# Performance work log

Measured on AMD Instinct MI355X. Metric: run time of the kernel, lower is better.

## Reference

```python
import jax, jax.numpy as jnp
import numpy as np

TAIL_BOUND = 20.0  # B
NUM_BINS = 16      # K
G, I = 8, 64       # n_gaussians, n_inputs
BATCH = 16384


def _rqs_forward(x, W, H, D, B):
    """Monotonic rational-quadratic spline (Durkan et al.), forward direction.
    x: [Bt,G,I]; W,H: [G,I,K] logits; D: [G,I,K-1] raw derivatives.
    Matches torch module: widths/heights = 2*B*softmax(logits), derivs = softplus,
    boundary derivatives fixed to 1, identity outside [-B, B].
    """
    dt = x.dtype
    widths = 2.0 * B * jax.nn.softmax(W, axis=-1)          # [G,I,K], sums to 2B
    heights = 2.0 * B * jax.nn.softmax(H, axis=-1)
    g, i, K = widths.shape
    one = jnp.ones((g, i, 1), dt)
    derivs = jnp.concatenate([one, jax.nn.softplus(D), one], axis=-1)  # [G,I,K+1]
    negB = jnp.full((g, i, 1), -B, dt)
    cumw = jnp.concatenate([negB, -B + jnp.cumsum(widths, -1)], -1)    # [G,I,K+1] knot x
    cumh = jnp.concatenate([negB, -B + jnp.cumsum(heights, -1)], -1)   # [G,I,K+1] knot y
    delta = heights / widths                                            # bin slopes

    inside = (x >= -B) & (x <= B)
    xc = jnp.clip(x, -B, B)
    # bin search: index of bin containing xc (broadcast compare vs. K+1 knots)
    idx = jnp.clip(jnp.sum((xc[..., None] >= cumw[None]).astype(jnp.int32), axis=-1) - 1, 0, K - 1)  # [Bt,G,I]

    gi = jnp.arange(g)[:, None]
    ii = jnp.arange(i)[None, :]

    def gather(p, j):  # p: [G,I,*], j: [Bt,G,I] -> [Bt,G,I]
        return p[gi, ii, j]

    in_cw, in_w = gather(cumw, idx), gather(widths, idx)
    in_ch, in_h = gather(cumh, idx), gather(heights, idx)
    in_delta = gather(delta, idx)
    d0, d1 = gather(derivs, idx), gather(derivs, idx + 1)

    theta = (xc - in_cw) / in_w
    tt = theta * (1.0 - theta)
    denom = in_delta + (d0 + d1 - 2.0 * in_delta) * tt
    numer = in_h * (in_delta * theta * theta + d0 * tt)
    z_in = in_ch + numer / denom
    dnum = in_delta * in_delta * (d1 * theta * theta + 2.0 * in_delta * tt + d0 * (1.0 - theta) ** 2)
    ld_in = jnp.log(dnum) - 2.0 * jnp.log(denom)

    z = jnp.where(inside, z_in, x)
    ld = jnp.where(inside, ld_in, jnp.zeros((), dt))
    return z, ld


def setup_inputs() -> dict:
    key = jax.random.key(0)
    kx, kw, kh, kd = jax.random.split(key, 4)
    # scale x so points spread across many bins; a few land outside the tail bound
    x = jax.random.normal(kx, (BATCH, G, I), dtype=jnp.float32) * 12.0
    W = jax.random.normal(kw, (G, I, NUM_BINS), dtype=jnp.float32)
    H = jax.random.normal(kh, (G, I, NUM_BINS), dtype=jnp.float32)
    D = jax.random.normal(kd, (G, I, NUM_BINS - 1), dtype=jnp.float32)
    return {"x": x, "W": W, "H": H, "D": D}


def reference(x, W, H, D):
    return _rqs_forward(x, W, H, D, TAIL_BOUND)
```

## Files before the change

### kernel.cpp

```cpp
#include <hip/hip_runtime.h>
#include <math.h>

#define TAIL_B 20.0f
#define BATCH 16384
#define NELEM (BATCH * 512)
#define ROWS_PB 64
#define LDS_BYTES 135168

typedef float vf4 __attribute__((ext_vector_type(4)));
typedef float vf2 __attribute__((ext_vector_type(2)));

__global__ __launch_bounds__(1024, 4) void rqs_fused(
    const float* __restrict__ x, const float* __restrict__ W,
    const float* __restrict__ H, const float* __restrict__ D,
    float* __restrict__ out)
{
    extern __shared__ float s[];
    float* sCW = s;
    float* sCH = s + 8704;
    vf2*   sDP = reinterpret_cast<vf2*>(s + 17408);

    const int tid   = threadIdx.x;
    const int col   = tid & 511;
    const int rsub  = tid >> 9;
    const int rbase = blockIdx.x * ROWS_PB + rsub * 32;
    const int csw   = col & 15;

    float xbA[8], xbB[8];
#pragma unroll
    for (int i = 0; i < 8; ++i)
        xbA[i] = x[(rbase + i) * 512 + col];

    {
        const int c    = tid >> 1;
        const int half = tid & 1;
        const float* Wg = W + c * 16 + half * 8;
        const float* Hg = H + c * 16 + half * 8;

        vf4 wa = *reinterpret_cast<const vf4*>(Wg);
        vf4 wb = *reinterpret_cast<const vf4*>(Wg + 4);
        vf4 ha = *reinterpret_cast<const vf4*>(Hg);
        vf4 hb = *reinterpret_cast<const vf4*>(Hg + 4);

        float mw = fmaxf(fmaxf(fmaxf(wa.x, wa.y), fmaxf(wa.z, wa.w)),
                         fmaxf(fmaxf(wb.x, wb.y), fmaxf(wb.z, wb.w)));
        float mh = fmaxf(fmaxf(fmaxf(ha.x, ha.y), fmaxf(ha.z, ha.w)),
                         fmaxf(fmaxf(hb.x, hb.y), fmaxf(hb.z, hb.w)));
        mw = fmaxf(mw, __shfl_xor(mw, 1));
        mh = fmaxf(mh, __shfl_xor(mh, 1));

        float ew[8] = {__expf(wa.x - mw), __expf(wa.y - mw), __expf(wa.z - mw), __expf(wa.w - mw),
                       __expf(wb.x - mw), __expf(wb.y - mw), __expf(wb.z - mw), __expf(wb.w - mw)};
        float eh[8] = {__expf(ha.x - mh), __expf(ha.y - mh), __expf(ha.z - mh), __expf(ha.w - mh),
                       __expf(hb.x - mh), __expf(hb.y - mh), __expf(hb.z - mh), __expf(hb.w - mh)};

        float sw = 0.0f, sh = 0.0f;
#pragma unroll
        for (int j = 0; j < 8; ++j) { sw += ew[j]; sh += eh[j]; }
        float swp = __shfl_xor(sw, 1), shp = __shfl_xor(sh, 1);
        float scw = (2.0f * TAIL_B) / (sw + swp);
        float sch = (2.0f * TAIL_B) / (sh + shp);

        float aw = half ? swp : 0.0f;
        float ah = half ? shp : 0.0f;

        const float* Dg = D + c * 15;
        float* cw = sCW + c * 17;
        float* ch = sCH + c * 17;
        vf2*   dp = sDP + c * 16;
        if (!half) { cw[0] = -TAIL_B; ch[0] = -TAIL_B; }

        float dk[9];
#pragma unroll
        for (int j = 0; j < 9; ++j) {
            int t = half * 8 + j;
            float dv = 1.0f;
            if (t >= 1 && t < 16) {
                float v = Dg[t - 1];
                dv = fmaxf(v, 0.0f) + __logf(1.0f + __expf(-fabsf(v)));
            }
            dk[j] = dv;
        }

#pragma unroll
        for (int j = 0; j < 8; ++j) {
            aw += ew[j]; ah += eh[j];
            int t = half * 8 + j + 1;
            cw[t] = -TAIL_B + aw * scw;
            ch[t] = -TAIL_B + ah * sch;
            int k = half * 8 + j;
            dp[k ^ (c & 15)] = (vf2){dk[j], dk[j + 1]};
        }
    }
    __syncthreads();

    float kr[15];
#pragma unroll
    for (int t = 0; t < 15; ++t) kr[t] = sCW[col * 17 + 1 + t];

    auto compute8 = [&](const float (&xb)[8], int r0) {
#pragma unroll
        for (int i = 0; i < 8; ++i) {
            float xx = xb[i];
            bool  inside = (xx >= -TAIL_B) && (xx <= TAIL_B);
            float xc = fminf(fmaxf(xx, -TAIL_B), TAIL_B);

            int idx = 0;
#pragma unroll
            for (int t = 0; t < 15; ++t) idx += (xc >= kr[t]) ? 1 : 0;

            int p = col * 17 + idx;
            float k0  = sCW[p], k1  = sCW[p + 1];
            float ch0 = sCH[p], ch1 = sCH[p + 1];
            vf2   dd  = sDP[col * 16 + (idx ^ csw)];
            float d0 = dd.x, d1 = dd.y;

            float invw  = __builtin_amdgcn_rcpf(k1 - k0);
            float hh    = ch1 - ch0;
            float de    = hh * invw;
            float theta = (xc - k0) * invw;
            float omt   = 1.0f - theta;
            float tt    = theta * omt;
            float denom = de + (d0 + d1 - 2.0f * de) * tt;
            float rden  = __builtin_amdgcn_rcpf(denom);
            float numer = hh * (de * theta * theta + d0 * tt);
            float zin   = ch0 + numer * rden;
            float dnum  = de * de * (d1 * theta * theta + 2.0f * de * tt + d0 * omt * omt);
            float ldin  = 0.6931471805599453f * __log2f(dnum * rden * rden);

            float z  = inside ? zin : xx;
            float ld = inside ? ldin : 0.0f;

            int addr = (r0 + i) * 512 + col;
            out[addr]         = z;
            out[NELEM + addr] = ld;
        }
    };

#pragma unroll
    for (int i = 0; i < 8; ++i) xbB[i] = x[(rbase + 8 + i) * 512 + col];
    compute8(xbA, rbase);

#pragma unroll
    for (int i = 0; i < 8; ++i) xbA[i] = x[(rbase + 16 + i) * 512 + col];
    compute8(xbB, rbase + 8);

#pragma unroll
    for (int i = 0; i < 8; ++i) xbB[i] = x[(rbase + 24 + i) * 512 + col];
    compute8(xbA, rbase + 16);

    compute8(xbB, rbase + 24);
}

extern "C" void kernel_launch(void* const* d_in, const int* in_sizes, int n_in,
                              void* d_out, int out_size, void* d_ws, size_t ws_size,
                              hipStream_t stream)
{
    const float* x = (const float*)d_in[0];
    const float* W = (const float*)d_in[1];
    const float* H = (const float*)d_in[2];
    const float* D = (const float*)d_in[3];
    float* out = (float*)d_out;

    hipFuncSetAttribute(reinterpret_cast<const void*>(&rqs_fused),
                        hipFuncAttributeMaxDynamicSharedMemorySize, LDS_BYTES);

    rqs_fused<<<BATCH / ROWS_PB, 1024, LDS_BYTES, stream>>>(x, W, H, D, out);
}
```

Measured before the change: 27.51 us.

## Process two columns per thread with float2 loads and nontemporal stores

Each thread now handles two adjacent columns, using 8-byte vector loads of x and 8-byte nontemporal stores of z and logdet. Rows are interleaved across four row slots instead of contiguous 32-row chunks. The aim is fewer, wider memory instructions and less cache pollution from the streaming output. In exchange each thread keeps two 15-entry knot arrays in registers, which raises register pressure and may hurt occupancy under the 1024x4 launch bounds.

Result: slower. 29.13 us (+5.9%).

```diff
diff --git a/kernel.cpp b/kernel.cpp
--- a/kernel.cpp
+++ b/kernel.cpp
@@ -21,15 +21,15 @@
     vf2*   sDP = reinterpret_cast<vf2*>(s + 17408);
 
     const int tid   = threadIdx.x;
-    const int col   = tid & 511;
-    const int rsub  = tid >> 9;
-    const int rbase = blockIdx.x * ROWS_PB + rsub * 32;
-    const int csw   = col & 15;
+    const int c2    = tid & 255;
+    const int cb    = c2 * 2;
+    const int rslot = tid >> 8;
+    const int rbase = blockIdx.x * ROWS_PB + rslot;
 
-    float xbA[8], xbB[8];
+    vf2 xA[4], xB[4];
 #pragma unroll
-    for (int i = 0; i < 8; ++i)
-        xbA[i] = x[(rbase + i) * 512 + col];
+    for (int i = 0; i < 4; ++i)
+        xA[i] = *reinterpret_cast<const vf2*>(x + (rbase + 4 * i) * 512 + cb);
 
     {
         const int c    = tid >> 1;
@@ -94,62 +94,75 @@
     }
     __syncthreads();
 
-    float kr[15];
+    float kr0[15], kr1[15];
 #pragma unroll
-    for (int t = 0; t < 15; ++t) kr[t] = sCW[col * 17 + 1 + t];
+    for (int t = 0; t < 15; ++t) kr0[t] = sCW[cb * 17 + 1 + t];
+#pragma unroll
+    for (int t = 0; t < 15; ++t) kr1[t] = sCW[(cb + 1) * 17 + 1 + t];
+    const int csw0 = cb & 15;
+    const int csw1 = (cb + 1) & 15;
 
-    auto compute8 = [&](const float (&xb)[8], int r0) {
+    auto evalc = [&](float xx, const float (&kr)[15], int col, int csw,
+                     float& z, float& ld) {
+        bool  inside = (xx >= -TAIL_B) && (xx <= TAIL_B);
+        float xc = fminf(fmaxf(xx, -TAIL_B), TAIL_B);
+        int idx = 0;
 #pragma unroll
-        for (int i = 0; i < 8; ++i) {
-            float xx = xb[i];
-            bool  inside = (xx >= -TAIL_B) && (xx <= TAIL_B);
-            float xc = fminf(fmaxf(xx, -TAIL_B), TAIL_B);
+        for (int t = 0; t < 15; ++t) idx += (xc >= kr[t]) ? 1 : 0;
 
-            int idx = 0;
+        int p = col * 17 + idx;
+        float k0  = sCW[p], k1  = sCW[p + 1];
+        float ch0 = sCH[p], ch1 = sCH[p + 1];
+        vf2   dd  = sDP[col * 16 + (idx ^ csw)];
+        float d0 = dd.x, d1 = dd.y;
+
+        float invw  = __builtin_amdgcn_rcpf(k1 - k0);
+        float hh    = ch1 - ch0;
+        float de    = hh * invw;
+        float theta = (xc - k0) * invw;
+        float omt   = 1.0f - theta;
+        float tt    = theta * omt;
+        float denom = de + (d0 + d1 - 2.0f * de) * tt;
+        float rden  = __builtin_amdgcn_rcpf(denom);
+        float numer = hh * (de * theta * theta + d0 * tt);
+        float zin   = ch0 + numer * rden;
+        float dnum  = de * de * (d1 * theta * theta + 2.0f * de * tt + d0 * omt * omt);
+        float ldin  = 0.6931471805599453f * __log2f(dnum * rden * rden);
+
+        z  = inside ? zin : xx;
+        ld = inside ? ldin : 0.0f;
+    };
+
+    auto compute4 = [&](const vf2 (&xv)[4], int c) {
 #pragma unroll
-            for (int t = 0; t < 15; ++t) idx += (xc >= kr[t]) ? 1 : 0;
-
-            int p = col * 17 + idx;
-            float k0  = sCW[p], k1  = sCW[p + 1];
-            float ch0 = sCH[p], ch1 = sCH[p + 1];
-            vf2   dd  = sDP[col * 16 + (idx ^ csw)];
-            float d0 = dd.x, d1 = dd.y;
-
-            float invw  = __builtin_amdgcn_rcpf(k1 - k0);
-            float hh    = ch1 - ch0;
-            float de    = hh * invw;
-            float theta = (xc - k0) * invw;
-            float omt   = 1.0f - theta;
-            float tt    = theta * omt;
-            float denom = de + (d0 + d1 - 2.0f * de) * tt;
-            float rden  = __builtin_amdgcn_rcpf(denom);
-            float numer = hh * (de * theta * theta + d0 * tt);
-            float zin   = ch0 + numer * rden;
-            float dnum  = de * de * (d1 * theta * theta + 2.0f * de * tt + d0 * omt * omt);
-            float ldin  = 0.6931471805599453f * __log2f(dnum * rden * rden);
-
-            float z  = inside ? zin : xx;
-            float ld = inside ? ldin : 0.0f;
-
-            int addr = (r0 + i) * 512 + col;
-            out[addr]         = z;
-            out[NELEM + addr] = ld;
+        for (int i = 0; i < 4; ++i) {
+            int r = rbase + 16 * c + 4 * i;
+            float z0, l0, z1, l1;
+            evalc(xv[i].x, kr0, cb,     csw0, z0, l0);
+            evalc(xv[i].y, kr1, cb + 1, csw1, z1, l1);
+            vf2 zq = {z0, z1};
+            vf2 lq = {l0, l1};
+            __builtin_nontemporal_store(zq, reinterpret_cast<vf2*>(out + r * 512 + cb));
+            __builtin_nontemporal_store(lq, reinterpret_cast<vf2*>(out + NELEM + r * 512 + cb));
         }
     };
 
 #pragma unroll
-    for (int i = 0; i < 8; ++i) xbB[i] = x[(rbase + 8 + i) * 512 + col];
-    compute8(xbA, rbase);
+    for (int i = 0; i < 4; ++i)
+        xB[i] = *reinterpret_cast<const vf2*>(x + (rbase + 16 + 4 * i) * 512 + cb);
+    compute4(xA, 0);
 
 #pragma unroll
-    for (int i = 0; i < 8; ++i) xbA[i] = x[(rbase + 16 + i) * 512 + col];
-    compute8(xbB, rbase + 8);
+    for (int i = 0; i < 4; ++i)
+        xA[i] = *reinterpret_cast<const vf2*>(x + (rbase + 32 + 4 * i) * 512 + cb);
+    compute4(xB, 1);
 
 #pragma unroll
-    for (int i = 0; i < 8; ++i) xbB[i] = x[(rbase + 24 + i) * 512 + col];
-    compute8(xbA, rbase + 16);
+    for (int i = 0; i < 4; ++i)
+        xB[i] = *reinterpret_cast<const vf2*>(x + (rbase + 48 + 4 * i) * 512 + cb);
+    compute4(xA, 2);
 
-    compute8(xbB, rbase + 24);
+    compute4(xB, 3);
 }
 
 extern "C" void kernel_launch(void* const* d_in, const int* in_sizes, int n_in,
```
